# Kernel tuning notes

Hardware: AMD Instinct MI355X
Metric: run time of the kernel (lower is better)

The kernel has to match this reference:

```python
import jax, jax.numpy as jnp
import numpy as np

B, S, H = 2, 1024, 2048          # batch, seq, hidden_size
I = 7168                          # intermediate_size
E = 8                             # num_local_experts
TOPK = 2                          # num_experts_per_tok
R = int(I * H * 0.1 / (I + H))    # delta_low_rank = 159


def setup_inputs() -> dict:
    key = jax.random.key(0)
    ks = jax.random.split(key, 12)
    s = 0.02
    return {
        "hidden_states": jax.random.normal(ks[0], (B, S, H), jnp.float32),
        "gate_w": jax.random.normal(ks[1], (E, H), jnp.float32) * s,
        "W1": jax.random.normal(ks[2], (E, I, H), jnp.float32) * s,
        "W2": jax.random.normal(ks[3], (E, H, I), jnp.float32) * s,
        "W3": jax.random.normal(ks[4], (E, I, H), jnp.float32) * s,
        "U1": jax.random.normal(ks[5], (E, I, R), jnp.float32) * s,
        "V1": jax.random.normal(ks[6], (E, R, H), jnp.float32) * s,
        "U2": jax.random.normal(ks[7], (E, H, R), jnp.float32) * s,
        "V2": jax.random.normal(ks[8], (E, R, I), jnp.float32) * s,
        "U3": jax.random.normal(ks[9], (E, I, R), jnp.float32) * s,
        "V3": jax.random.normal(ks[10], (E, R, H), jnp.float32) * s,
    }


def reference(hidden_states, gate_w, W1, W2, W3, U1, V1, U2, V2, U3, V3):
    b, s, h = hidden_states.shape
    x = hidden_states.reshape(-1, h)                     # [T, H]
    T = x.shape[0]
    router_logits = x @ gate_w.T                          # [T, E]
    probs = jax.nn.softmax(router_logits.astype(jnp.float32), axis=-1)
    rw, sel = jax.lax.top_k(probs, TOPK)                  # [T, k]
    rw = rw / jnp.sum(rw, axis=-1, keepdims=True)
    rw = rw.astype(x.dtype)
    # dense combine weights: zero for unselected experts (same math as gather/scatter)
    comb = jnp.zeros((T, E), x.dtype).at[jnp.arange(T)[:, None], sel].add(rw)
    out = jnp.zeros_like(x)
    for e in range(E):                                    # small fixed expert loop
        up = x @ W3[e].T + (x @ V3[e].T) @ U3[e].T        # [T, I]
        gate = x @ W1[e].T + (x @ V1[e].T) @ U1[e].T      # [T, I]
        hmid = jax.nn.silu(gate) * up                     # [T, I]
        y = hmid @ W2[e].T + (hmid @ V2[e].T) @ U2[e].T   # [T, H]
        out = out + comb[:, e, None] * y
    return out.reshape(b, s, h), router_logits
```

## Files before the change

### kernel.cpp

```cpp
#include <hip/hip_runtime.h>
#include <cstdint>
#include <cstddef>

#define TT 2048
#define HH 2048
#define II 7168
#define EE 8
#define RR 159
#define RPAD 192
#define ROWS 4096

typedef __attribute__((ext_vector_type(8))) short bf16x8;
typedef __attribute__((ext_vector_type(4))) float f32x4;

__device__ __forceinline__ unsigned short f2bf(float f) {
  unsigned int u = __float_as_uint(f);
  u += 0x7fffu + ((u >> 16) & 1u);
  return (unsigned short)(u >> 16);
}
__device__ __forceinline__ float bf2f(unsigned short u) {
  return __uint_as_float(((unsigned int)u) << 16);
}
__device__ __forceinline__ unsigned int cvtpk(float lo, float hi) {
  unsigned int r;
  asm volatile("v_cvt_pk_bf16_f32 %0, %1, %2" : "=v"(r) : "v"(lo), "v"(hi));
  return r;
}
__device__ __forceinline__ bf16x8 zero8() {
  bf16x8 v;
#pragma unroll
  for (int j = 0; j < 8; j++) v[j] = 0;
  return v;
}
__device__ __forceinline__ void gload16(const unsigned short* g, unsigned short* l) {
  __builtin_amdgcn_global_load_lds(
      (const __attribute__((address_space(1))) unsigned int*)g,
      (__attribute__((address_space(3))) unsigned int*)l, 16, 0, 0);
}

__global__ __launch_bounds__(256) void k_f2bf_flat(const float* __restrict__ s,
                                                   unsigned short* __restrict__ d,
                                                   long long n8) {
  long long i = (long long)blockIdx.x * blockDim.x + threadIdx.x;
  long long stride = (long long)gridDim.x * blockDim.x;
  for (; i < n8; i += stride) {
    const float* p = s + i * 8;
    float4 a = *(const float4*)p;
    float4 b = *(const float4*)(p + 4);
    bf16x8 v;
    v[0] = (short)f2bf(a.x); v[1] = (short)f2bf(a.y);
    v[2] = (short)f2bf(a.z); v[3] = (short)f2bf(a.w);
    v[4] = (short)f2bf(b.x); v[5] = (short)f2bf(b.y);
    v[6] = (short)f2bf(b.z); v[7] = (short)f2bf(b.w);
    *(bf16x8*)(d + i * 8) = v;
  }
}

__global__ __launch_bounds__(256) void k_upad(const float* __restrict__ U,
                                              unsigned short* __restrict__ Up, int rows) {
  long long idx = (long long)blockIdx.x * 256 + threadIdx.x;
  long long total = (long long)rows * 24;
  if (idx >= total) return;
  int row = (int)(idx / 24), c8 = (int)(idx % 24);
  unsigned short* dp = Up + (size_t)row * RPAD + c8 * 8;
#pragma unroll
  for (int j = 0; j < 8; j++) {
    int c = c8 * 8 + j;
    dp[j] = (c < RR) ? f2bf(U[(size_t)row * RR + c]) : (unsigned short)0;
  }
}

__global__ __launch_bounds__(256) void k_router(
    const float* __restrict__ x, const float* __restrict__ gw,
    float* __restrict__ logits_out, int* __restrict__ sel,
    float* __restrict__ wtok, int* __restrict__ counts,
    unsigned short* __restrict__ xb) {
  int t = blockIdx.x;
  const float* xr = x + (size_t)t * HH;
  int base = threadIdx.x * 8;
  float4 x0 = *(const float4*)(xr + base);
  float4 x1 = *(const float4*)(xr + base + 4);
  {
    bf16x8 v;
    v[0] = (short)f2bf(x0.x); v[1] = (short)f2bf(x0.y);
    v[2] = (short)f2bf(x0.z); v[3] = (short)f2bf(x0.w);
    v[4] = (short)f2bf(x1.x); v[5] = (short)f2bf(x1.y);
    v[6] = (short)f2bf(x1.z); v[7] = (short)f2bf(x1.w);
    *(bf16x8*)(xb + (size_t)t * HH + base) = v;
  }
  float part[EE];
#pragma unroll
  for (int e = 0; e < EE; e++) {
    const float* g = gw + (size_t)e * HH + base;
    float4 g0 = *(const float4*)g;
    float4 g1 = *(const float4*)(g + 4);
    part[e] = x0.x * g0.x + x0.y * g0.y + x0.z * g0.z + x0.w * g0.w +
              x1.x * g1.x + x1.y * g1.y + x1.z * g1.z + x1.w * g1.w;
  }
#pragma unroll
  for (int off = 32; off > 0; off >>= 1)
#pragma unroll
    for (int e = 0; e < EE; e++) part[e] += __shfl_down(part[e], off);
  __shared__ float red[4][EE];
  int w = threadIdx.x >> 6, lane = threadIdx.x & 63;
  if (lane == 0) {
#pragma unroll
    for (int e = 0; e < EE; e++) red[w][e] = part[e];
  }
  __syncthreads();
  if (threadIdx.x == 0) {
    float lg[EE];
    float mx = -1e30f;
#pragma unroll
    for (int e = 0; e < EE; e++) {
      lg[e] = red[0][e] + red[1][e] + red[2][e] + red[3][e];
      logits_out[(size_t)t * EE + e] = lg[e];
      mx = fmaxf(mx, lg[e]);
    }
    float p[EE];
#pragma unroll
    for (int e = 0; e < EE; e++) p[e] = __expf(lg[e] - mx);
    int i0 = 0;
#pragma unroll
    for (int e = 1; e < EE; e++)
      if (lg[e] > lg[i0]) i0 = e;
    int i1 = (i0 == 0) ? 1 : 0;
#pragma unroll
    for (int e = 0; e < EE; e++)
      if (e != i0 && lg[e] > lg[i1]) i1 = e;
    float s = p[i0] + p[i1];
    sel[t * 2] = i0;
    sel[t * 2 + 1] = i1;
    wtok[t * 2] = p[i0] / s;
    wtok[t * 2 + 1] = p[i1] / s;
    atomicAdd(&counts[i0], 1);
    atomicAdd(&counts[i1], 1);
  }
}

__global__ void k_offsets(const int* __restrict__ counts, int* __restrict__ offs,
                          int* __restrict__ curs) {
  if (threadIdx.x == 0 && blockIdx.x == 0) {
    int o = 0;
    for (int e = 0; e < EE; e++) {
      offs[e] = o;
      curs[e] = o;
      o += counts[e];
    }
    offs[EE] = o;
  }
}

__global__ void k_build(const int* __restrict__ sel, const float* __restrict__ wtok,
                        int* __restrict__ curs, int* __restrict__ rowsA,
                        float* __restrict__ rowwgt, int* __restrict__ rowid) {
  int t = blockIdx.x * blockDim.x + threadIdx.x;
  if (t >= TT) return;
  for (int k = 0; k < 2; k++) {
    int e = sel[t * 2 + k];
    int pos = atomicAdd(&curs[e], 1);
    rowsA[pos] = t;
    rowwgt[pos] = wtok[t * 2 + k];
    rowid[t * 2 + k] = pos;
  }
}

template <bool GATHER>
__global__ __launch_bounds__(256, 2) void k_lowrank_sk(
    const unsigned short* __restrict__ Ab, int lda, int K, int kc, int NS,
    const unsigned short* __restrict__ V0, const unsigned short* __restrict__ V1,
    float* __restrict__ Pp,
    const int* __restrict__ counts, const int* __restrict__ offs,
    const int* __restrict__ rowsA) {
  int e = blockIdx.y;
  int cnt = counts[e];
  int m0 = blockIdx.x * 64;
  if (m0 >= cnt) return;
  int roff = offs[e];
  int mat = blockIdx.z / NS, split = blockIdx.z % NS;
  const unsigned short* V = ((mat == 0) ? V0 : V1) + (size_t)e * RR * K;
  float* Pout = Pp + (size_t)blockIdx.z * ROWS * RPAD;
  int kt0 = split * kc;
  int kt1 = kt0 + kc;
  if (kt1 > K) kt1 = K;
  __shared__ unsigned short As[64 * 64];
  __shared__ unsigned short Bs[192 * 64];
  int tid = threadIdx.x, lane = tid & 63, w = tid >> 6;
  int rstage = tid >> 3, cg = tid & 7;
  f32x4 acc[12];
#pragma unroll
  for (int n = 0; n < 12; n++) acc[n] = (f32x4){0.f, 0.f, 0.f, 0.f};
  for (int kt = kt0; kt < kt1; kt += 64) {
#pragma unroll
    for (int p = 0; p < 2; p++) {
      int r = p * 32 + rstage;
      bf16x8 v = zero8();
      int gr = m0 + r;
      if (gr < cnt) {
        size_t arow = GATHER ? (size_t)rowsA[roff + gr] : (size_t)(roff + gr);
        v = *(const bf16x8*)(Ab + arow * (size_t)lda + kt + cg * 8);
      }
      *(bf16x8*)&As[r * 64 + ((cg ^ (r & 7)) * 8)] = v;
    }
#pragma unroll
    for (int p = 0; p < 6; p++) {
      int r = p * 32 + rstage;
      bf16x8 v = zero8();
      if (r < RR) v = *(const bf16x8*)(V + (size_t)r * K + kt + cg * 8);
      *(bf16x8*)&Bs[r * 64 + ((cg ^ (r & 7)) * 8)] = v;
    }
    __syncthreads();
#pragma unroll
    for (int ks = 0; ks < 2; ks++) {
      int rA = w * 16 + (lane & 15);
      bf16x8 a = *(const bf16x8*)&As[rA * 64 + (((ks * 4 + (lane >> 4)) ^ (rA & 7)) * 8)];
#pragma unroll
      for (int n = 0; n < 12; n++) {
        int rB = n * 16 + (lane & 15);
        bf16x8 b = *(const bf16x8*)&Bs[rB * 64 + (((ks * 4 + (lane >> 4)) ^ (rB & 7)) * 8)];
        acc[n] = __builtin_amdgcn_mfma_f32_16x16x32_bf16(a, b, acc[n], 0, 0, 0);
      }
    }
    __syncthreads();
  }
  int mbase = m0 + w * 16 + (lane >> 4) * 4;
#pragma unroll
  for (int n = 0; n < 12; n++) {
    int col = n * 16 + (lane & 15);
#pragma unroll
    for (int r4 = 0; r4 < 4; r4++) {
      int row = mbase + r4;
      if (row < cnt) Pout[(size_t)(roff + row) * RPAD + col] = acc[n][r4];
    }
  }
}

__global__ __launch_bounds__(256) void k_lr_reduce(
    const float* __restrict__ Pp, unsigned short* __restrict__ P0,
    unsigned short* __restrict__ P1m, int NS, int nmat) {
  long long idx = (long long)blockIdx.x * 256 + threadIdx.x;
  long long total = (long long)nmat * ROWS * 24;
  if (idx >= total) return;
  int mat = (int)(idx / ((long long)ROWS * 24));
  int rem = (int)(idx % ((long long)ROWS * 24));
  int row = rem / 24, c8 = rem % 24;
  const float* base = Pp + ((size_t)mat * NS) * ROWS * RPAD + (size_t)row * RPAD + c8 * 8;
  float s0 = 0, s1 = 0, s2 = 0, s3 = 0, s4 = 0, s5 = 0, s6 = 0, s7 = 0;
  for (int sp = 0; sp < NS; sp++) {
    const float* p = base + (size_t)sp * ROWS * RPAD;
    float4 a = *(const float4*)p;
    float4 b = *(const float4*)(p + 4);
    s0 += a.x; s1 += a.y; s2 += a.z; s3 += a.w;
    s4 += b.x; s5 += b.y; s6 += b.z; s7 += b.w;
  }
  bf16x8 v;
  v[0] = (short)f2bf(s0); v[1] = (short)f2bf(s1);
  v[2] = (short)f2bf(s2); v[3] = (short)f2bf(s3);
  v[4] = (short)f2bf(s4); v[5] = (short)f2bf(s5);
  v[6] = (short)f2bf(s6); v[7] = (short)f2bf(s7);
  unsigned short* P = (mat == 0) ? P0 : P1m;
  *(bf16x8*)(P + (size_t)row * RPAD + c8 * 8) = v;
}

template <int MODE>
__global__ __launch_bounds__(256, 2) void k_gemm(
    const unsigned short* __restrict__ Ab, int K, int N,
    const float* __restrict__ Wf,
    const unsigned short* __restrict__ Pq,
    const unsigned short* __restrict__ Uq,
    const unsigned short* __restrict__ Gb,
    const float* __restrict__ rowwgt,
    unsigned short* __restrict__ outb,
    float* __restrict__ outf,
    const int* __restrict__ counts, const int* __restrict__ offs,
    const int* __restrict__ rowsA) {
  int e = blockIdx.z;
  int cnt = counts[e];
  int m0 = blockIdx.y * 128;
  if (m0 >= cnt) return;
  int n0 = blockIdx.x * 128;
  int roff = offs[e];
  const float* w = Wf + (size_t)e * (size_t)N * K;
  const unsigned short* uq = Uq + (size_t)e * (size_t)N * RPAD;
  __shared__ unsigned short As[2][128 * 64];
  __shared__ unsigned short Bs[128 * 64];
  int tid = threadIdx.x, lane = tid & 63, wv = tid >> 6;
  int wr = (wv >> 1) * 64, wc = (wv & 1) * 64;
  f32x4 acc[4][4];
#pragma unroll
  for (int m = 0; m < 4; m++)
#pragma unroll
    for (int n = 0; n < 4; n++) acc[m][n] = (f32x4){0.f, 0.f, 0.f, 0.f};
  int srow = (wv << 5) + (lane >> 3);
  int swz = (((lane & 7) ^ ((lane >> 3) & 7)) << 3);
  int aoff[4], woff[4];
#pragma unroll
  for (int i = 0; i < 4; i++) {
    int gr = m0 + srow + i * 8;
    if (gr >= cnt) gr = cnt - 1;
    int arow = (MODE < 2) ? rowsA[roff + gr] : (roff + gr);
    aoff[i] = arow * K + swz;
    woff[i] = (n0 + srow + i * 8) * K + swz;
  }
  float4 rb[4][2];
#pragma unroll
  for (int i = 0; i < 4; i++) {
    gload16(Ab + aoff[i], &As[0][((wv << 5) + (i << 3)) * 64]);
    rb[i][0] = *(const float4*)(w + woff[i]);
    rb[i][1] = *(const float4*)(w + woff[i] + 4);
  }
  int nt = K >> 6;
  for (int t = 0; t < nt; ++t) {
    int cur = t & 1, nxt = cur ^ 1;
#pragma unroll
    for (int i = 0; i < 4; i++) {
      int idx = (srow + i * 8) * 64 + (lane & 7) * 8;
      uint4 q;
      q.x = cvtpk(rb[i][0].x, rb[i][0].y);
      q.y = cvtpk(rb[i][0].z, rb[i][0].w);
      q.z = cvtpk(rb[i][1].x, rb[i][1].y);
      q.w = cvtpk(rb[i][1].z, rb[i][1].w);
      *(uint4*)&Bs[idx] = q;
    }
    __syncthreads();
    bool more = (t + 1 < nt);
    if (more) {
#pragma unroll
      for (int i = 0; i < 4; i++) {
        gload16(Ab + aoff[i] + (t + 1) * 64, &As[nxt][((wv << 5) + (i << 3)) * 64]);
        rb[i][0] = *(const float4*)(w + woff[i] + (t + 1) * 64);
        rb[i][1] = *(const float4*)(w + woff[i] + (t + 1) * 64 + 4);
      }
    }
#pragma unroll
    for (int ks = 0; ks < 2; ks++) {
      bf16x8 af[4], bsr[4];
#pragma unroll
      for (int m = 0; m < 4; m++) {
        int r = wr + m * 16 + (lane & 15);
        af[m] = *(const bf16x8*)&As[cur][r * 64 + (((ks * 4 + (lane >> 4)) ^ (r & 7)) * 8)];
      }
#pragma unroll
      for (int n = 0; n < 4; n++) {
        int r = wc + n * 16 + (lane & 15);
        bsr[n] = *(const bf16x8*)&Bs[r * 64 + (((ks * 4 + (lane >> 4)) ^ (r & 7)) * 8)];
      }
#pragma unroll
      for (int m = 0; m < 4; m++)
#pragma unroll
        for (int n = 0; n < 4; n++)
          acc[m][n] = __builtin_amdgcn_mfma_f32_16x16x32_bf16(af[m], bsr[n], acc[m][n], 0, 0, 0);
    }
    __syncthreads();
  }
  for (int kt = 0; kt < RPAD; kt += 64) {
#pragma unroll
    for (int i = 0; i < 4; i++) {
      int gr = m0 + srow + i * 8;
      if (gr >= cnt) gr = cnt - 1;
      gload16(Pq + (size_t)(roff + gr) * RPAD + swz + kt, &As[0][((wv << 5) + (i << 3)) * 64]);
      gload16(uq + (size_t)(n0 + srow + i * 8) * RPAD + swz + kt,
              &Bs[((wv << 5) + (i << 3)) * 64]);
    }
    __syncthreads();
#pragma unroll
    for (int ks = 0; ks < 2; ks++) {
      bf16x8 af[4], bsr[4];
#pragma unroll
      for (int m = 0; m < 4; m++) {
        int r = wr + m * 16 + (lane & 15);
        af[m] = *(const bf16x8*)&As[0][r * 64 + (((ks * 4 + (lane >> 4)) ^ (r & 7)) * 8)];
      }
#pragma unroll
      for (int n = 0; n < 4; n++) {
        int r = wc + n * 16 + (lane & 15);
        bsr[n] = *(const bf16x8*)&Bs[r * 64 + (((ks * 4 + (lane >> 4)) ^ (r & 7)) * 8)];
      }
#pragma unroll
      for (int m = 0; m < 4; m++)
#pragma unroll
        for (int n = 0; n < 4; n++)
          acc[m][n] = __builtin_amdgcn_mfma_f32_16x16x32_bf16(af[m], bsr[n], acc[m][n], 0, 0, 0);
    }
    __syncthreads();
  }
#pragma unroll
  for (int m = 0; m < 4; m++) {
#pragma unroll
    for (int r4 = 0; r4 < 4; r4++) {
      int row = m0 + wr + m * 16 + (lane >> 4) * 4 + r4;
      if (row < cnt) {
        size_t rbase = (size_t)(roff + row) * N + n0 + wc;
        if constexpr (MODE == 0) {
#pragma unroll
          for (int n = 0; n < 4; n++)
            outb[rbase + n * 16 + (lane & 15)] = f2bf(acc[m][n][r4]);
        } else if constexpr (MODE == 1) {
#pragma unroll
          for (int n = 0; n < 4; n++) {
            float g = bf2f(Gb[rbase + n * 16 + (lane & 15)]);
            float uu = acc[m][n][r4];
            float h = (g / (1.f + __expf(-g))) * uu;
            outb[rbase + n * 16 + (lane & 15)] = f2bf(h);
          }
        } else {
          float wgt = rowwgt[roff + row];
#pragma unroll
          for (int n = 0; n < 4; n++)
            outf[rbase + n * 16 + (lane & 15)] = acc[m][n][r4] * wgt;
        }
      }
    }
  }
}

__global__ void k_combine(const float* __restrict__ ybuf, const int* __restrict__ rowid,
                          float* __restrict__ out) {
  int idx = blockIdx.x * 256 + threadIdx.x;
  int t = idx >> 8;
  int c = (idx & 255) * 8;
  int r0 = rowid[t * 2], r1 = rowid[t * 2 + 1];
  const float* y0 = ybuf + (size_t)r0 * HH + c;
  const float* y1 = ybuf + (size_t)r1 * HH + c;
  float4 a0 = *(const float4*)y0, a1 = *(const float4*)(y0 + 4);
  float4 b0 = *(const float4*)y1, b1 = *(const float4*)(y1 + 4);
  float4 o0 = {a0.x + b0.x, a0.y + b0.y, a0.z + b0.z, a0.w + b0.w};
  float4 o1 = {a1.x + b1.x, a1.y + b1.y, a1.z + b1.z, a1.w + b1.w};
  float* o = out + (size_t)t * HH + c;
  *(float4*)o = o0;
  *(float4*)(o + 4) = o1;
}

extern "C" void kernel_launch(void* const* d_in, const int* in_sizes, int n_in,
                              void* d_out, int out_size, void* d_ws, size_t ws_size,
                              hipStream_t stream) {
  const float* x  = (const float*)d_in[0];
  const float* gw = (const float*)d_in[1];
  const float* W1 = (const float*)d_in[2];
  const float* W2 = (const float*)d_in[3];
  const float* W3 = (const float*)d_in[4];
  const float* U1 = (const float*)d_in[5];
  const float* V1 = (const float*)d_in[6];
  const float* U2 = (const float*)d_in[7];
  const float* V2 = (const float*)d_in[8];
  const float* U3 = (const float*)d_in[9];
  const float* V3 = (const float*)d_in[10];
  float* out = (float*)d_out;
  float* logits = out + (size_t)TT * HH;

  char* ws = (char*)d_ws;
  size_t off = 0;
  auto take = [&](size_t b) -> char* {
    char* p = ws + off;
    off += (b + 255) & ~(size_t)255;
    return p;
  };
  unsigned short* Xb   = (unsigned short*)take((size_t)TT * HH * 2);
  unsigned short* hmid = (unsigned short*)take((size_t)ROWS * II * 2);
  unsigned short* Gbuf = (unsigned short*)take((size_t)ROWS * II * 2);
  unsigned short* P1   = (unsigned short*)take((size_t)ROWS * RPAD * 2);
  unsigned short* P3   = (unsigned short*)take((size_t)ROWS * RPAD * 2);
  unsigned short* P2   = (unsigned short*)take((size_t)ROWS * RPAD * 2);
  float* ybuf          = (float*)take((size_t)ROWS * HH * 4);
  int* sel             = (int*)take((size_t)TT * 2 * 4);
  float* wtok          = (float*)take((size_t)TT * 2 * 4);
  int* rowsA           = (int*)take((size_t)ROWS * 4);
  float* rowwgt        = (float*)take((size_t)ROWS * 4);
  int* rowid           = (int*)take((size_t)TT * 2 * 4);
  int* meta            = (int*)take(1024);
  int* counts  = meta;
  int* offs    = meta + 16;
  int* curs    = meta + 32;
  unsigned short* V1b = (unsigned short*)take((size_t)EE * RR * HH * 2);
  unsigned short* V3b = (unsigned short*)take((size_t)EE * RR * HH * 2);
  unsigned short* V2b = (unsigned short*)take((size_t)EE * RR * II * 2);
  unsigned short* U1p = (unsigned short*)take((size_t)EE * II * RPAD * 2);
  unsigned short* U3p = (unsigned short*)take((size_t)EE * II * RPAD * 2);
  unsigned short* U2p = (unsigned short*)take((size_t)EE * HH * RPAD * 2);
  float* Pp           = (float*)take((size_t)8 * ROWS * RPAD * 4);

  hipMemsetAsync(counts, 0, EE * sizeof(int), stream);
  k_f2bf_flat<<<1024, 256, 0, stream>>>(V1, V1b, (long long)EE * RR * HH / 8);
  k_f2bf_flat<<<1024, 256, 0, stream>>>(V3, V3b, (long long)EE * RR * HH / 8);
  k_f2bf_flat<<<1024, 256, 0, stream>>>(V2, V2b, (long long)EE * RR * II / 8);
  k_upad<<<(EE * II * 24 + 255) / 256, 256, 0, stream>>>(U1, U1p, EE * II);
  k_upad<<<(EE * II * 24 + 255) / 256, 256, 0, stream>>>(U3, U3p, EE * II);
  k_upad<<<(EE * HH * 24 + 255) / 256, 256, 0, stream>>>(U2, U2p, EE * HH);
  k_router<<<TT, 256, 0, stream>>>(x, gw, logits, sel, wtok, counts, Xb);
  k_offsets<<<1, 64, 0, stream>>>(counts, offs, curs);
  k_build<<<TT / 256, 256, 0, stream>>>(sel, wtok, curs, rowsA, rowwgt, rowid);
  k_lowrank_sk<true><<<dim3(TT / 64, EE, 2 * 4), 256, 0, stream>>>(
      Xb, HH, HH, 512, 4, V1b, V3b, Pp, counts, offs, rowsA);
  k_lr_reduce<<<(2 * ROWS * 24 + 255) / 256, 256, 0, stream>>>(Pp, P1, P3, 4, 2);
  k_gemm<0><<<dim3(II / 128, TT / 128, EE), 256, 0, stream>>>(
      Xb, HH, II, W1, P1, U1p, nullptr, nullptr, Gbuf, nullptr, counts, offs, rowsA);
  k_gemm<1><<<dim3(II / 128, TT / 128, EE), 256, 0, stream>>>(
      Xb, HH, II, W3, P3, U3p, Gbuf, nullptr, hmid, nullptr, counts, offs, rowsA);
  k_lowrank_sk<false><<<dim3(TT / 64, EE, 8), 256, 0, stream>>>(
      hmid, II, II, 896, 8, V2b, V2b, Pp, counts, offs, rowsA);
  k_lr_reduce<<<(ROWS * 24 + 255) / 256, 256, 0, stream>>>(Pp, P2, P2, 8, 1);
  k_gemm<2><<<dim3(HH / 128, TT / 128, EE), 256, 0, stream>>>(
      hmid, II, HH, W2, P2, U2p, nullptr, rowwgt, nullptr, ybuf, counts, offs, rowsA);
  k_combine<<<(TT * HH / 8) / 256, 256, 0, stream>>>(ybuf, rowid, out);
}
```

Baseline: 1.197 ms.

## Merge low-rank deltas into dense bf16 weights and fuse gate/up GEMMs

Precomputes W+U·V for all three projections per call into bf16 weight buffers, removing the separate low-rank projection, split-K reduction and correction passes. The gate and up projections are fused into one kernel that applies SiLU·up in the epilogue, and the down projection becomes a plain GEMM. In exchange, the merge reads all fp32 weights and writes a full bf16 copy every call, and the new GEMMs drop the previous double-buffered prefetch.

```diff
diff --git a/kernel.cpp b/kernel.cpp
--- a/kernel.cpp
+++ b/kernel.cpp
@@ -20,11 +20,6 @@
 }
 __device__ __forceinline__ float bf2f(unsigned short u) {
   return __uint_as_float(((unsigned int)u) << 16);
-}
-__device__ __forceinline__ unsigned int cvtpk(float lo, float hi) {
-  unsigned int r;
-  asm volatile("v_cvt_pk_bf16_f32 %0, %1, %2" : "=v"(r) : "v"(lo), "v"(hi));
-  return r;
 }
 __device__ __forceinline__ bf16x8 zero8() {
   bf16x8 v;
@@ -67,6 +62,82 @@
   for (int j = 0; j < 8; j++) {
     int c = c8 * 8 + j;
     dp[j] = (c < RR) ? f2bf(U[(size_t)row * RR + c]) : (unsigned short)0;
+  }
+}
+
+__global__ __launch_bounds__(256, 2) void k_merge(
+    const float* __restrict__ Wf, const unsigned short* __restrict__ Upad,
+    const unsigned short* __restrict__ Vb, unsigned short* __restrict__ Wb,
+    int M2, int C) {
+  int e = blockIdx.z;
+  int row0 = blockIdx.y * 128;
+  int col0 = blockIdx.x * 128;
+  const float* w = Wf + (size_t)e * M2 * C;
+  const unsigned short* up = Upad + (size_t)e * M2 * RPAD;
+  const unsigned short* vb = Vb + (size_t)e * RR * C;
+  unsigned short* wb = Wb + (size_t)e * M2 * C;
+  __shared__ unsigned short Us[128 * 64];
+  __shared__ unsigned short Vt[128 * 72];
+  int tid = threadIdx.x, lane = tid & 63, wv = tid >> 6;
+  int wr = (wv >> 1) * 64, wc = (wv & 1) * 64;
+  int rstage = tid >> 3, cg = tid & 7;
+  f32x4 acc[4][4];
+#pragma unroll
+  for (int m = 0; m < 4; m++)
+#pragma unroll
+    for (int n = 0; n < 4; n++) acc[m][n] = (f32x4){0.f, 0.f, 0.f, 0.f};
+  int rl = tid & 15;
+  int h8 = (tid >> 4) * 8;
+  for (int kt = 0; kt < RPAD; kt += 64) {
+#pragma unroll
+    for (int p = 0; p < 4; p++) {
+      int r = p * 32 + rstage;
+      bf16x8 v = *(const bf16x8*)(up + (size_t)(row0 + r) * RPAD + kt + cg * 8);
+      *(bf16x8*)&Us[r * 64 + ((cg ^ (r & 7)) * 8)] = v;
+    }
+#pragma unroll
+    for (int rr = 0; rr < 4; rr++) {
+      int r = rr * 16 + rl;
+      int rg = kt + r;
+      bf16x8 v = zero8();
+      if (rg < RR) v = *(const bf16x8*)(vb + (size_t)rg * C + col0 + h8);
+#pragma unroll
+      for (int j = 0; j < 8; j++) Vt[(h8 + j) * 72 + r] = (unsigned short)v[j];
+    }
+    __syncthreads();
+#pragma unroll
+    for (int ks = 0; ks < 2; ks++) {
+      bf16x8 af[4], bf[4];
+#pragma unroll
+      for (int m = 0; m < 4; m++) {
+        int r = wr + m * 16 + (lane & 15);
+        af[m] = *(const bf16x8*)&Us[r * 64 + (((ks * 4 + (lane >> 4)) ^ (r & 7)) * 8)];
+      }
+#pragma unroll
+      for (int n = 0; n < 4; n++) {
+        int h = wc + n * 16 + (lane & 15);
+        bf[n] = *(const bf16x8*)&Vt[h * 72 + (ks * 4 + (lane >> 4)) * 8];
+      }
+#pragma unroll
+      for (int m = 0; m < 4; m++)
+#pragma unroll
+        for (int n = 0; n < 4; n++)
+          acc[m][n] = __builtin_amdgcn_mfma_f32_16x16x32_bf16(af[m], bf[n], acc[m][n], 0, 0, 0);
+    }
+    __syncthreads();
+  }
+#pragma unroll
+  for (int m = 0; m < 4; m++) {
+#pragma unroll
+    for (int r4 = 0; r4 < 4; r4++) {
+      int row = row0 + wr + m * 16 + (lane >> 4) * 4 + r4;
+#pragma unroll
+      for (int n = 0; n < 4; n++) {
+        int col = col0 + wc + n * 16 + (lane & 15);
+        size_t idx = (size_t)row * C + col;
+        wb[idx] = f2bf(w[idx] + acc[m][n][r4]);
+      }
+    }
   }
 }
 
@@ -165,113 +236,10 @@
   }
 }
 
-template <bool GATHER>
-__global__ __launch_bounds__(256, 2) void k_lowrank_sk(
-    const unsigned short* __restrict__ Ab, int lda, int K, int kc, int NS,
-    const unsigned short* __restrict__ V0, const unsigned short* __restrict__ V1,
-    float* __restrict__ Pp,
-    const int* __restrict__ counts, const int* __restrict__ offs,
-    const int* __restrict__ rowsA) {
-  int e = blockIdx.y;
-  int cnt = counts[e];
-  int m0 = blockIdx.x * 64;
-  if (m0 >= cnt) return;
-  int roff = offs[e];
-  int mat = blockIdx.z / NS, split = blockIdx.z % NS;
-  const unsigned short* V = ((mat == 0) ? V0 : V1) + (size_t)e * RR * K;
-  float* Pout = Pp + (size_t)blockIdx.z * ROWS * RPAD;
-  int kt0 = split * kc;
-  int kt1 = kt0 + kc;
-  if (kt1 > K) kt1 = K;
-  __shared__ unsigned short As[64 * 64];
-  __shared__ unsigned short Bs[192 * 64];
-  int tid = threadIdx.x, lane = tid & 63, w = tid >> 6;
-  int rstage = tid >> 3, cg = tid & 7;
-  f32x4 acc[12];
-#pragma unroll
-  for (int n = 0; n < 12; n++) acc[n] = (f32x4){0.f, 0.f, 0.f, 0.f};
-  for (int kt = kt0; kt < kt1; kt += 64) {
-#pragma unroll
-    for (int p = 0; p < 2; p++) {
-      int r = p * 32 + rstage;
-      bf16x8 v = zero8();
-      int gr = m0 + r;
-      if (gr < cnt) {
-        size_t arow = GATHER ? (size_t)rowsA[roff + gr] : (size_t)(roff + gr);
-        v = *(const bf16x8*)(Ab + arow * (size_t)lda + kt + cg * 8);
-      }
-      *(bf16x8*)&As[r * 64 + ((cg ^ (r & 7)) * 8)] = v;
-    }
-#pragma unroll
-    for (int p = 0; p < 6; p++) {
-      int r = p * 32 + rstage;
-      bf16x8 v = zero8();
-      if (r < RR) v = *(const bf16x8*)(V + (size_t)r * K + kt + cg * 8);
-      *(bf16x8*)&Bs[r * 64 + ((cg ^ (r & 7)) * 8)] = v;
-    }
-    __syncthreads();
-#pragma unroll
-    for (int ks = 0; ks < 2; ks++) {
-      int rA = w * 16 + (lane & 15);
-      bf16x8 a = *(const bf16x8*)&As[rA * 64 + (((ks * 4 + (lane >> 4)) ^ (rA & 7)) * 8)];
-#pragma unroll
-      for (int n = 0; n < 12; n++) {
-        int rB = n * 16 + (lane & 15);
-        bf16x8 b = *(const bf16x8*)&Bs[rB * 64 + (((ks * 4 + (lane >> 4)) ^ (rB & 7)) * 8)];
-        acc[n] = __builtin_amdgcn_mfma_f32_16x16x32_bf16(a, b, acc[n], 0, 0, 0);
-      }
-    }
-    __syncthreads();
-  }
-  int mbase = m0 + w * 16 + (lane >> 4) * 4;
-#pragma unroll
-  for (int n = 0; n < 12; n++) {
-    int col = n * 16 + (lane & 15);
-#pragma unroll
-    for (int r4 = 0; r4 < 4; r4++) {
-      int row = mbase + r4;
-      if (row < cnt) Pout[(size_t)(roff + row) * RPAD + col] = acc[n][r4];
-    }
-  }
-}
-
-__global__ __launch_bounds__(256) void k_lr_reduce(
-    const float* __restrict__ Pp, unsigned short* __restrict__ P0,
-    unsigned short* __restrict__ P1m, int NS, int nmat) {
-  long long idx = (long long)blockIdx.x * 256 + threadIdx.x;
-  long long total = (long long)nmat * ROWS * 24;
-  if (idx >= total) return;
-  int mat = (int)(idx / ((long long)ROWS * 24));
-  int rem = (int)(idx % ((long long)ROWS * 24));
-  int row = rem / 24, c8 = rem % 24;
-  const float* base = Pp + ((size_t)mat * NS) * ROWS * RPAD + (size_t)row * RPAD + c8 * 8;
-  float s0 = 0, s1 = 0, s2 = 0, s3 = 0, s4 = 0, s5 = 0, s6 = 0, s7 = 0;
-  for (int sp = 0; sp < NS; sp++) {
-    const float* p = base + (size_t)sp * ROWS * RPAD;
-    float4 a = *(const float4*)p;
-    float4 b = *(const float4*)(p + 4);
-    s0 += a.x; s1 += a.y; s2 += a.z; s3 += a.w;
-    s4 += b.x; s5 += b.y; s6 += b.z; s7 += b.w;
-  }
-  bf16x8 v;
-  v[0] = (short)f2bf(s0); v[1] = (short)f2bf(s1);
-  v[2] = (short)f2bf(s2); v[3] = (short)f2bf(s3);
-  v[4] = (short)f2bf(s4); v[5] = (short)f2bf(s5);
-  v[6] = (short)f2bf(s6); v[7] = (short)f2bf(s7);
-  unsigned short* P = (mat == 0) ? P0 : P1m;
-  *(bf16x8*)(P + (size_t)row * RPAD + c8 * 8) = v;
-}
-
-template <int MODE>
-__global__ __launch_bounds__(256, 2) void k_gemm(
-    const unsigned short* __restrict__ Ab, int K, int N,
-    const float* __restrict__ Wf,
-    const unsigned short* __restrict__ Pq,
-    const unsigned short* __restrict__ Uq,
-    const unsigned short* __restrict__ Gb,
-    const float* __restrict__ rowwgt,
-    unsigned short* __restrict__ outb,
-    float* __restrict__ outf,
+__global__ __launch_bounds__(256, 2) void k_mlp1(
+    const unsigned short* __restrict__ Xb,
+    const unsigned short* __restrict__ W1b, const unsigned short* __restrict__ W3b,
+    unsigned short* __restrict__ hmid,
     const int* __restrict__ counts, const int* __restrict__ offs,
     const int* __restrict__ rowsA) {
   int e = blockIdx.z;
@@ -280,107 +248,66 @@
   if (m0 >= cnt) return;
   int n0 = blockIdx.x * 128;
   int roff = offs[e];
-  const float* w = Wf + (size_t)e * (size_t)N * K;
-  const unsigned short* uq = Uq + (size_t)e * (size_t)N * RPAD;
-  __shared__ unsigned short As[2][128 * 64];
-  __shared__ unsigned short Bs[128 * 64];
-  int tid = threadIdx.x, lane = tid & 63, wv = tid >> 6;
-  int wr = (wv >> 1) * 64, wc = (wv & 1) * 64;
-  f32x4 acc[4][4];
+  __shared__ unsigned short As[128 * 64];
+  __shared__ unsigned short Bg[128 * 64];
+  __shared__ unsigned short Bu[128 * 64];
+  int tid = threadIdx.x, lane = tid & 63, w = tid >> 6;
+  int wr = (w >> 1) * 64, wc = (w & 1) * 64;
+  f32x4 accg[4][4], accu[4][4];
 #pragma unroll
   for (int m = 0; m < 4; m++)
 #pragma unroll
-    for (int n = 0; n < 4; n++) acc[m][n] = (f32x4){0.f, 0.f, 0.f, 0.f};
-  int srow = (wv << 5) + (lane >> 3);
+    for (int n = 0; n < 4; n++) {
+      accg[m][n] = (f32x4){0.f, 0.f, 0.f, 0.f};
+      accu[m][n] = (f32x4){0.f, 0.f, 0.f, 0.f};
+    }
+  int srow = (w << 5) + (lane >> 3);
   int swz = (((lane & 7) ^ ((lane >> 3) & 7)) << 3);
-  int aoff[4], woff[4];
-#pragma unroll
-  for (int i = 0; i < 4; i++) {
-    int gr = m0 + srow + i * 8;
-    if (gr >= cnt) gr = cnt - 1;
-    int arow = (MODE < 2) ? rowsA[roff + gr] : (roff + gr);
-    aoff[i] = arow * K + swz;
-    woff[i] = (n0 + srow + i * 8) * K + swz;
-  }
-  float4 rb[4][2];
-#pragma unroll
-  for (int i = 0; i < 4; i++) {
-    gload16(Ab + aoff[i], &As[0][((wv << 5) + (i << 3)) * 64]);
-    rb[i][0] = *(const float4*)(w + woff[i]);
-    rb[i][1] = *(const float4*)(w + woff[i] + 4);
-  }
-  int nt = K >> 6;
-  for (int t = 0; t < nt; ++t) {
-    int cur = t & 1, nxt = cur ^ 1;
-#pragma unroll
-    for (int i = 0; i < 4; i++) {
-      int idx = (srow + i * 8) * 64 + (lane & 7) * 8;
-      uint4 q;
-      q.x = cvtpk(rb[i][0].x, rb[i][0].y);
-      q.y = cvtpk(rb[i][0].z, rb[i][0].w);
-      q.z = cvtpk(rb[i][1].x, rb[i][1].y);
-      q.w = cvtpk(rb[i][1].z, rb[i][1].w);
-      *(uint4*)&Bs[idx] = q;
-    }
-    __syncthreads();
-    bool more = (t + 1 < nt);
-    if (more) {
-#pragma unroll
-      for (int i = 0; i < 4; i++) {
-        gload16(Ab + aoff[i] + (t + 1) * 64, &As[nxt][((wv << 5) + (i << 3)) * 64]);
-        rb[i][0] = *(const float4*)(w + woff[i] + (t + 1) * 64);
-        rb[i][1] = *(const float4*)(w + woff[i] + (t + 1) * 64 + 4);
-      }
-    }
-#pragma unroll
-    for (int ks = 0; ks < 2; ks++) {
-      bf16x8 af[4], bsr[4];
-#pragma unroll
-      for (int m = 0; m < 4; m++) {
-        int r = wr + m * 16 + (lane & 15);
-        af[m] = *(const bf16x8*)&As[cur][r * 64 + (((ks * 4 + (lane >> 4)) ^ (r & 7)) * 8)];
-      }
-#pragma unroll
-      for (int n = 0; n < 4; n++) {
-        int r = wc + n * 16 + (lane & 15);
-        bsr[n] = *(const bf16x8*)&Bs[r * 64 + (((ks * 4 + (lane >> 4)) ^ (r & 7)) * 8)];
-      }
-#pragma unroll
-      for (int m = 0; m < 4; m++)
-#pragma unroll
-        for (int n = 0; n < 4; n++)
-          acc[m][n] = __builtin_amdgcn_mfma_f32_16x16x32_bf16(af[m], bsr[n], acc[m][n], 0, 0, 0);
-    }
-    __syncthreads();
-  }
-  for (int kt = 0; kt < RPAD; kt += 64) {
+  const unsigned short* pa[4];
+  const unsigned short* pg[4];
+  const unsigned short* pu[4];
+  {
+    const unsigned short* w1 = W1b + (size_t)e * II * HH;
+    const unsigned short* w3 = W3b + (size_t)e * II * HH;
 #pragma unroll
     for (int i = 0; i < 4; i++) {
       int gr = m0 + srow + i * 8;
       if (gr >= cnt) gr = cnt - 1;
-      gload16(Pq + (size_t)(roff + gr) * RPAD + swz + kt, &As[0][((wv << 5) + (i << 3)) * 64]);
-      gload16(uq + (size_t)(n0 + srow + i * 8) * RPAD + swz + kt,
-              &Bs[((wv << 5) + (i << 3)) * 64]);
+      pa[i] = Xb + (size_t)rowsA[roff + gr] * HH + swz;
+      pg[i] = w1 + (size_t)(n0 + srow + i * 8) * HH + swz;
+      pu[i] = w3 + (size_t)(n0 + srow + i * 8) * HH + swz;
+    }
+  }
+  for (int kt = 0; kt < HH; kt += 64) {
+#pragma unroll
+    for (int i = 0; i < 4; i++) {
+      gload16(pa[i] + kt, &As[((w << 5) + (i << 3)) * 64]);
+      gload16(pg[i] + kt, &Bg[((w << 5) + (i << 3)) * 64]);
+      gload16(pu[i] + kt, &Bu[((w << 5) + (i << 3)) * 64]);
     }
     __syncthreads();
 #pragma unroll
     for (int ks = 0; ks < 2; ks++) {
-      bf16x8 af[4], bsr[4];
+      bf16x8 af[4], bg[4], bu[4];
 #pragma unroll
       for (int m = 0; m < 4; m++) {
         int r = wr + m * 16 + (lane & 15);
-        af[m] = *(const bf16x8*)&As[0][r * 64 + (((ks * 4 + (lane >> 4)) ^ (r & 7)) * 8)];
+        af[m] = *(const bf16x8*)&As[r * 64 + (((ks * 4 + (lane >> 4)) ^ (r & 7)) * 8)];
       }
 #pragma unroll
       for (int n = 0; n < 4; n++) {
         int r = wc + n * 16 + (lane & 15);
-        bsr[n] = *(const bf16x8*)&Bs[r * 64 + (((ks * 4 + (lane >> 4)) ^ (r & 7)) * 8)];
+        int idx = r * 64 + (((ks * 4 + (lane >> 4)) ^ (r & 7)) * 8);
+        bg[n] = *(const bf16x8*)&Bg[idx];
+        bu[n] = *(const bf16x8*)&Bu[idx];
       }
 #pragma unroll
       for (int m = 0; m < 4; m++)
 #pragma unroll
-        for (int n = 0; n < 4; n++)
-          acc[m][n] = __builtin_amdgcn_mfma_f32_16x16x32_bf16(af[m], bsr[n], acc[m][n], 0, 0, 0);
+        for (int n = 0; n < 4; n++) {
+          accg[m][n] = __builtin_amdgcn_mfma_f32_16x16x32_bf16(af[m], bg[n], accg[m][n], 0, 0, 0);
+          accu[m][n] = __builtin_amdgcn_mfma_f32_16x16x32_bf16(af[m], bu[n], accu[m][n], 0, 0, 0);
+        }
     }
     __syncthreads();
   }
@@ -390,25 +317,91 @@
     for (int r4 = 0; r4 < 4; r4++) {
       int row = m0 + wr + m * 16 + (lane >> 4) * 4 + r4;
       if (row < cnt) {
-        size_t rbase = (size_t)(roff + row) * N + n0 + wc;
-        if constexpr (MODE == 0) {
-#pragma unroll
-          for (int n = 0; n < 4; n++)
-            outb[rbase + n * 16 + (lane & 15)] = f2bf(acc[m][n][r4]);
-        } else if constexpr (MODE == 1) {
-#pragma unroll
-          for (int n = 0; n < 4; n++) {
-            float g = bf2f(Gb[rbase + n * 16 + (lane & 15)]);
-            float uu = acc[m][n][r4];
-            float h = (g / (1.f + __expf(-g))) * uu;
-            outb[rbase + n * 16 + (lane & 15)] = f2bf(h);
-          }
-        } else {
-          float wgt = rowwgt[roff + row];
-#pragma unroll
-          for (int n = 0; n < 4; n++)
-            outf[rbase + n * 16 + (lane & 15)] = acc[m][n][r4] * wgt;
+        size_t rb = (size_t)(roff + row) * II + n0 + wc;
+#pragma unroll
+        for (int n = 0; n < 4; n++) {
+          float g = accg[m][n][r4], uu = accu[m][n][r4];
+          float h = (g / (1.f + __expf(-g))) * uu;
+          hmid[rb + n * 16 + (lane & 15)] = f2bf(h);
         }
+      }
+    }
+  }
+}
+
+__global__ __launch_bounds__(256, 2) void k_mlp2(
+    const unsigned short* __restrict__ hmid,
+    const unsigned short* __restrict__ W2b,
+    const float* __restrict__ rowwgt, float* __restrict__ ybuf,
+    const int* __restrict__ counts, const int* __restrict__ offs) {
+  int e = blockIdx.z;
+  int cnt = counts[e];
+  int m0 = blockIdx.y * 128;
+  if (m0 >= cnt) return;
+  int n0 = blockIdx.x * 128;
+  int roff = offs[e];
+  __shared__ unsigned short As[128 * 64];
+  __shared__ unsigned short Bs[128 * 64];
+  int tid = threadIdx.x, lane = tid & 63, w = tid >> 6;
+  int wr = (w >> 1) * 64, wc = (w & 1) * 64;
+  f32x4 acc[4][4];
+#pragma unroll
+  for (int m = 0; m < 4; m++)
+#pragma unroll
+    for (int n = 0; n < 4; n++) acc[m][n] = (f32x4){0.f, 0.f, 0.f, 0.f};
+  int srow = (w << 5) + (lane >> 3);
+  int swz = (((lane & 7) ^ ((lane >> 3) & 7)) << 3);
+  const unsigned short* pa[4];
+  const unsigned short* pb[4];
+  {
+    const unsigned short* w2 = W2b + (size_t)e * HH * II;
+#pragma unroll
+    for (int i = 0; i < 4; i++) {
+      int gr = m0 + srow + i * 8;
+      if (gr >= cnt) gr = cnt - 1;
+      pa[i] = hmid + (size_t)(roff + gr) * II + swz;
+      pb[i] = w2 + (size_t)(n0 + srow + i * 8) * II + swz;
+    }
+  }
+  for (int kt = 0; kt < II; kt += 64) {
+#pragma unroll
+    for (int i = 0; i < 4; i++) {
+      gload16(pa[i] + kt, &As[((w << 5) + (i << 3)) * 64]);
+      gload16(pb[i] + kt, &Bs[((w << 5) + (i << 3)) * 64]);
+    }
+    __syncthreads();
+#pragma unroll
+    for (int ks = 0; ks < 2; ks++) {
+      bf16x8 af[4], bs[4];
+#pragma unroll
+      for (int m = 0; m < 4; m++) {
+        int r = wr + m * 16 + (lane & 15);
+        af[m] = *(const bf16x8*)&As[r * 64 + (((ks * 4 + (lane >> 4)) ^ (r & 7)) * 8)];
+      }
+#pragma unroll
+      for (int n = 0; n < 4; n++) {
+        int r = wc + n * 16 + (lane & 15);
+        bs[n] = *(const bf16x8*)&Bs[r * 64 + (((ks * 4 + (lane >> 4)) ^ (r & 7)) * 8)];
+      }
+#pragma unroll
+      for (int m = 0; m < 4; m++)
+#pragma unroll
+        for (int n = 0; n < 4; n++)
+          acc[m][n] = __builtin_amdgcn_mfma_f32_16x16x32_bf16(af[m], bs[n], acc[m][n], 0, 0, 0);
+    }
+    __syncthreads();
+  }
+#pragma unroll
+  for (int m = 0; m < 4; m++) {
+#pragma unroll
+    for (int r4 = 0; r4 < 4; r4++) {
+      int row = m0 + wr + m * 16 + (lane >> 4) * 4 + r4;
+      if (row < cnt) {
+        float wgt = rowwgt[roff + row];
+        size_t rb = (size_t)(roff + row) * HH + n0 + wc;
+#pragma unroll
+        for (int n = 0; n < 4; n++)
+          ybuf[rb + n * 16 + (lane & 15)] = acc[m][n][r4] * wgt;
       }
     }
   }
@@ -457,10 +450,6 @@
   };
   unsigned short* Xb   = (unsigned short*)take((size_t)TT * HH * 2);
   unsigned short* hmid = (unsigned short*)take((size_t)ROWS * II * 2);
-  unsigned short* Gbuf = (unsigned short*)take((size_t)ROWS * II * 2);
-  unsigned short* P1   = (unsigned short*)take((size_t)ROWS * RPAD * 2);
-  unsigned short* P3   = (unsigned short*)take((size_t)ROWS * RPAD * 2);
-  unsigned short* P2   = (unsigned short*)take((size_t)ROWS * RPAD * 2);
   float* ybuf          = (float*)take((size_t)ROWS * HH * 4);
   int* sel             = (int*)take((size_t)TT * 2 * 4);
   float* wtok          = (float*)take((size_t)TT * 2 * 4);
@@ -471,13 +460,15 @@
   int* counts  = meta;
   int* offs    = meta + 16;
   int* curs    = meta + 32;
+  unsigned short* W1b = (unsigned short*)take((size_t)EE * II * HH * 2);
+  unsigned short* W3b = (unsigned short*)take((size_t)EE * II * HH * 2);
+  unsigned short* W2b = (unsigned short*)take((size_t)EE * HH * II * 2);
   unsigned short* V1b = (unsigned short*)take((size_t)EE * RR * HH * 2);
   unsigned short* V3b = (unsigned short*)take((size_t)EE * RR * HH * 2);
   unsigned short* V2b = (unsigned short*)take((size_t)EE * RR * II * 2);
   unsigned short* U1p = (unsigned short*)take((size_t)EE * II * RPAD * 2);
   unsigned short* U3p = (unsigned short*)take((size_t)EE * II * RPAD * 2);
   unsigned short* U2p = (unsigned short*)take((size_t)EE * HH * RPAD * 2);
-  float* Pp           = (float*)take((size_t)8 * ROWS * RPAD * 4);
 
   hipMemsetAsync(counts, 0, EE * sizeof(int), stream);
   k_f2bf_flat<<<1024, 256, 0, stream>>>(V1, V1b, (long long)EE * RR * HH / 8);
@@ -486,20 +477,15 @@
   k_upad<<<(EE * II * 24 + 255) / 256, 256, 0, stream>>>(U1, U1p, EE * II);
   k_upad<<<(EE * II * 24 + 255) / 256, 256, 0, stream>>>(U3, U3p, EE * II);
   k_upad<<<(EE * HH * 24 + 255) / 256, 256, 0, stream>>>(U2, U2p, EE * HH);
+  k_merge<<<dim3(HH / 128, II / 128, EE), 256, 0, stream>>>(W1, U1p, V1b, W1b, II, HH);
+  k_merge<<<dim3(HH / 128, II / 128, EE), 256, 0, stream>>>(W3, U3p, V3b, W3b, II, HH);
+  k_merge<<<dim3(II / 128, HH / 128, EE), 256, 0, stream>>>(W2, U2p, V2b, W2b, HH, II);
   k_router<<<TT, 256, 0, stream>>>(x, gw, logits, sel, wtok, counts, Xb);
   k_offsets<<<1, 64, 0, stream>>>(counts, offs, curs);
   k_build<<<TT / 256, 256, 0, stream>>>(sel, wtok, curs, rowsA, rowwgt, rowid);
-  k_lowrank_sk<true><<<dim3(TT / 64, EE, 2 * 4), 256, 0, stream>>>(
-      Xb, HH, HH, 512, 4, V1b, V3b, Pp, counts, offs, rowsA);
-  k_lr_reduce<<<(2 * ROWS * 24 + 255) / 256, 256, 0, stream>>>(Pp, P1, P3, 4, 2);
-  k_gemm<0><<<dim3(II / 128, TT / 128, EE), 256, 0, stream>>>(
-      Xb, HH, II, W1, P1, U1p, nullptr, nullptr, Gbuf, nullptr, counts, offs, rowsA);
-  k_gemm<1><<<dim3(II / 128, TT / 128, EE), 256, 0, stream>>>(
-      Xb, HH, II, W3, P3, U3p, Gbuf, nullptr, hmid, nullptr, counts, offs, rowsA);
-  k_lowrank_sk<false><<<dim3(TT / 64, EE, 8), 256, 0, stream>>>(
-      hmid, II, II, 896, 8, V2b, V2b, Pp, counts, offs, rowsA);
-  k_lr_reduce<<<(ROWS * 24 + 255) / 256, 256, 0, stream>>>(Pp, P2, P2, 8, 1);
-  k_gemm<2><<<dim3(HH / 128, TT / 128, EE), 256, 0, stream>>>(
-      hmid, II, HH, W2, P2, U2p, nullptr, rowwgt, nullptr, ybuf, counts, offs, rowsA);
+  k_mlp1<<<dim3(II / 128, TT / 128, EE), 256, 0, stream>>>(
+      Xb, W1b, W3b, hmid, counts, offs, rowsA);
+  k_mlp2<<<dim3(HH / 128, TT / 128, EE), 256, 0, stream>>>(
+      hmid, W2b, rowwgt, ybuf, counts, offs);
   k_combine<<<(TT * HH / 8) / 256, 256, 0, stream>>>(ybuf, rowid, out);
 }
```

After: 1.293 ms. 1.08x slower.
